# Kernel optimization log

Hardware: AMD Instinct MI355X
Metric: run time of the kernel (lower is better)

## Reference

```python
import jax, jax.numpy as jnp
import numpy as np

N_NODES = 65536
N_EDGES = 524288
N_GRAPHS = 512
G_NODES = 10000
NUM_DISEASES = 2000
IN_DIM = 128
HID = 256  # 2 * IN_DIM (z_emb concat feat)
D_FEAT = 512
C_FEAT = 512
MAX_Z = 4000


def setup_inputs() -> dict:
    key = jax.random.key(0)
    ks = jax.random.split(key, 20)
    rn = lambda k, shape: jax.random.normal(k, shape, dtype=jnp.float32) * 0.05
    return {
        "z": jax.random.randint(ks[0], (N_NODES,), 0, MAX_Z),
        "node_id": jnp.sort(jax.random.randint(ks[1], (N_NODES,), 0, G_NODES)),
        "src": jax.random.randint(ks[2], (N_EDGES,), 0, N_NODES),
        "dst": jax.random.randint(ks[3], (N_EDGES,), 0, N_NODES),
        "graph_ids": jnp.sort(jax.random.randint(ks[4], (N_NODES,), 0, N_GRAPHS)),
        "z_table": rn(ks[5], (MAX_Z, IN_DIM)),
        "d_feat_tab": rn(ks[6], (G_NODES, D_FEAT)),
        "c_feat_tab": rn(ks[7], (G_NODES, C_FEAT)),
        "Wd": rn(ks[8], (D_FEAT, IN_DIM)),
        "Wc": rn(ks[9], (C_FEAT, IN_DIM)),
        "gin_W1": rn(ks[10], (HID, HID)), "gin_b1": jnp.zeros((HID,), jnp.float32),
        "gin_W2": rn(ks[11], (HID, HID)), "gin_b2": jnp.zeros((HID,), jnp.float32),
        "sage_Wself": rn(ks[12], (HID, HID)),
        "sage_Wneigh": rn(ks[13], (HID, HID)),
        "sage_b": jnp.zeros((HID,), jnp.float32),
        "lin1_W": rn(ks[14], (HID, HID)), "lin1_b": jnp.zeros((HID,), jnp.float32),
        "lin2_W": rn(ks[15], (HID, 1)), "lin2_b": jnp.zeros((1,), jnp.float32),
    }


def reference(z, node_id, src, dst, graph_ids, z_table, d_feat_tab, c_feat_tab,
              Wd, Wc, gin_W1, gin_b1, gin_W2, gin_b2,
              sage_Wself, sage_Wneigh, sage_b, lin1_W, lin1_b, lin2_W, lin2_b):
    # --- input feature construction (Model.forward) ---
    z_emb = z_table[z]                               # [N, IN_DIM]
    d_proj = d_feat_tab[node_id] @ Wd                # d_fc (bias=False)
    c_proj = c_feat_tab[node_id] @ Wc                # c_fc (bias=False)
    disease = (node_id <= NUM_DISEASES)[:, None]
    # node_id is sorted -> masked concat order == node order
    feat = jnp.where(disease, d_proj, c_proj)        # [N, IN_DIM]
    x = jnp.concatenate([z_emb, feat], axis=1)       # [N, HID]
    # --- GINConv: sum aggregation, eps=0, mlp = Lin->ReLU->Lin ---
    agg = jax.ops.segment_sum(x[src], dst, num_segments=N_NODES)
    h = x + agg
    h = jax.nn.relu(h @ gin_W1 + gin_b1) @ gin_W2 + gin_b2
    # --- SAGEConv('mean'): fc_self(h) + fc_neigh(mean_neighbors) + bias ---
    deg = jax.ops.segment_sum(jnp.ones((N_EDGES,), h.dtype), dst, num_segments=N_NODES)
    mean_n = jax.ops.segment_sum(h[src], dst, num_segments=N_NODES) / jnp.maximum(deg, 1.0)[:, None]
    h = h @ sage_Wself + mean_n @ sage_Wneigh + sage_b
    # --- per-graph max pooling readout ---
    g = jax.ops.segment_max(h, graph_ids, num_segments=N_GRAPHS, indices_are_sorted=True)
    g = jnp.where(jnp.isfinite(g), g, 0.0)           # guard empty graphs
    # --- head: Linear -> ReLU -> (dropout p=0, eval) -> Linear ---
    h = jax.nn.relu(g @ lin1_W + lin1_b)
    return h @ lin2_W + lin2_b                       # [N_GRAPHS, 1]
```

## Files before the change

kernel.cpp:

```cpp
#include <hip/hip_runtime.h>
#include <hip/hip_bf16.h>

#define N_NODES     65536
#define N_EDGES     524288
#define N_GRAPHS    512
#define G_NODES_N   10000
#define NUM_DIS     2000
#define IN_DIM      128
#define HID         256
#define D_FEAT      512
#define POOL_SPLIT  8

typedef _Float16 half8 __attribute__((ext_vector_type(8)));
typedef _Float16 half4v __attribute__((ext_vector_type(4)));
typedef float    f32x4 __attribute__((ext_vector_type(4)));

typedef __attribute__((address_space(1))) const void as1_void;
typedef __attribute__((address_space(3))) void       as3_void;

__global__ __launch_bounds__(256) void wcvt_all_kernel(
    const float* __restrict__ W1, const float* __restrict__ W2,
    const float* __restrict__ Ws, const float* __restrict__ Wn,
    const float* __restrict__ Wd, const float* __restrict__ Wc,
    _Float16* __restrict__ W1T, _Float16* __restrict__ W2T,
    _Float16* __restrict__ WsT, _Float16* __restrict__ WnT,
    _Float16* __restrict__ WdT, _Float16* __restrict__ WcT)
{
    __shared__ float tile[64][65];
    const int b = blockIdx.x;
    const int mat = b >> 4, t = b & 15;
    const float* W; _Float16* T; int K, N, k0, n0;
    if (mat < 4) {
        K = HID; N = HID; k0 = (t >> 2) * 64; n0 = (t & 3) * 64;
        W = (mat == 0) ? W1 : (mat == 1) ? W2 : (mat == 2) ? Ws : Wn;
        T = (mat == 0) ? W1T : (mat == 1) ? W2T : (mat == 2) ? WsT : WnT;
    } else {
        K = D_FEAT; N = IN_DIM; k0 = (t >> 1) * 64; n0 = (t & 1) * 64;
        W = (mat == 4) ? Wd : Wc;
        T = (mat == 4) ? WdT : WcT;
    }
    const int tx = threadIdx.x & 63, ty = threadIdx.x >> 6;
    #pragma unroll
    for (int r = 0; r < 64; r += 4)
        tile[r + ty][tx] = W[(size_t)(k0 + r + ty) * N + n0 + tx];
    __syncthreads();
    #pragma unroll
    for (int c = 0; c < 64; c += 4)
        T[(size_t)(n0 + c + ty) * K + k0 + tx] = (_Float16)tile[tx][c + ty];
}

__global__ __launch_bounds__(256) void proj_mfma_kernel(
    const float* __restrict__ dtab, const float* __restrict__ ctab,
    const _Float16* __restrict__ WdT, const _Float16* __restrict__ WcT,
    _Float16* __restrict__ proj)
{
    __shared__ _Float16 Alds[128 * 40];
    __shared__ _Float16 Blds[128 * 40];
    const int blk = blockIdx.x;
    const float* tab; const _Float16* WT; int base, M, bm;
    if (blk < 16) { tab = dtab; WT = WdT; base = 0;           M = NUM_DIS + 1;             bm = blk * 128; }
    else          { tab = ctab; WT = WcT; base = NUM_DIS + 1; M = G_NODES_N - NUM_DIS - 1; bm = (blk - 16) * 128; }
    const int tid  = threadIdx.x;
    const int wave = tid >> 6, lane = tid & 63;
    const int q    = lane >> 4, l16 = lane & 15;
    const int mbase = (wave & 1) * 64, nbase = (wave >> 1) * 64;
    const int r = tid >> 1, s = tid & 1;

    f32x4 acc[4][4] = {};

    for (int kc = 0; kc < 16; ++kc) {
        const int k0 = kc * 32;
        const int arow = min(bm + r, M - 1);
        const float* gA = tab + (size_t)(base + arow) * D_FEAT + k0 + s * 16;
        const _Float16* gB = WT + (size_t)r * D_FEAT + k0 + s * 16;
        const float4 f0 = ((const float4*)gA)[0];
        const float4 f1 = ((const float4*)gA)[1];
        const float4 f2 = ((const float4*)gA)[2];
        const float4 f3 = ((const float4*)gA)[3];
        const half8 hb0 = *(const half8*)gB;
        const half8 hb1 = *(const half8*)(gB + 8);
        half8 h0, h1;
        h0[0]=(_Float16)f0.x; h0[1]=(_Float16)f0.y; h0[2]=(_Float16)f0.z; h0[3]=(_Float16)f0.w;
        h0[4]=(_Float16)f1.x; h0[5]=(_Float16)f1.y; h0[6]=(_Float16)f1.z; h0[7]=(_Float16)f1.w;
        h1[0]=(_Float16)f2.x; h1[1]=(_Float16)f2.y; h1[2]=(_Float16)f2.z; h1[3]=(_Float16)f2.w;
        h1[4]=(_Float16)f3.x; h1[5]=(_Float16)f3.y; h1[6]=(_Float16)f3.z; h1[7]=(_Float16)f3.w;
        __syncthreads();
        *(half8*)&Alds[r * 40 + s * 16]     = h0;
        *(half8*)&Alds[r * 40 + s * 16 + 8] = h1;
        *(half8*)&Blds[r * 40 + s * 16]     = hb0;
        *(half8*)&Blds[r * 40 + s * 16 + 8] = hb1;
        __syncthreads();
        half8 a[4], b[4];
        #pragma unroll
        for (int i = 0; i < 4; ++i)
            a[i] = *(const half8*)&Alds[(mbase + i * 16 + l16) * 40 + q * 8];
        #pragma unroll
        for (int j = 0; j < 4; ++j)
            b[j] = *(const half8*)&Blds[(nbase + j * 16 + l16) * 40 + q * 8];
        #pragma unroll
        for (int i = 0; i < 4; ++i)
            #pragma unroll
            for (int j = 0; j < 4; ++j)
                acc[i][j] = __builtin_amdgcn_mfma_f32_16x16x32_f16(a[i], b[j], acc[i][j], 0, 0, 0);
    }

    #pragma unroll
    for (int j = 0; j < 4; ++j) {
        const int colg = nbase + j * 16 + l16;
        #pragma unroll
        for (int i = 0; i < 4; ++i) {
            #pragma unroll
            for (int rr = 0; rr < 4; ++rr) {
                const int row = bm + mbase + i * 16 + q * 4 + rr;
                if (row < M)
                    proj[(size_t)(base + row) * IN_DIM + colg] = (_Float16)acc[i][j][rr];
            }
        }
    }
}

__global__ __launch_bounds__(256) void build_x_kernel(
    const int* __restrict__ z, const int* __restrict__ node_id,
    const float* __restrict__ z_table, const _Float16* __restrict__ proj,
    _Float16* __restrict__ X)
{
    const int t = blockIdx.x * 256 + threadIdx.x;
    const int node = t >> 6;
    const int q    = t & 63;
    half4v h;
    if (q < 32) {
        const float4 v = ((const float4*)(z_table + (size_t)z[node] * IN_DIM))[q];
        h[0] = (_Float16)v.x; h[1] = (_Float16)v.y;
        h[2] = (_Float16)v.z; h[3] = (_Float16)v.w;
    } else {
        h = *(const half4v*)(proj + (size_t)node_id[node] * IN_DIM + (q - 32) * 4);
    }
    *(half4v*)(X + (size_t)node * HID + q * 4) = h;
}

__global__ __launch_bounds__(256) void hist_kernel(
    const int* __restrict__ dst, int* __restrict__ cnt)
{
    const int e = blockIdx.x * 256 + threadIdx.x;
    if (e < N_EDGES) atomicAdd(&cnt[dst[e]], 1);
}

__global__ __launch_bounds__(256) void seg_sum_kernel(
    const int* __restrict__ cnt, int* __restrict__ seg)
{
    __shared__ int red[256];
    const int t = threadIdx.x;
    const int4 c = *(const int4*)(cnt + blockIdx.x * 1024 + t * 4);
    red[t] = c.x + c.y + c.z + c.w;
    __syncthreads();
    for (int s = 128; s > 0; s >>= 1) {
        if (t < s) red[t] += red[t + s];
        __syncthreads();
    }
    if (t == 0) seg[blockIdx.x] = red[0];
}

__global__ __launch_bounds__(64) void seg_scan_kernel(
    const int* __restrict__ seg, int* __restrict__ segoff,
    int* __restrict__ total_out)
{
    __shared__ int a[64], b[64];
    const int t = threadIdx.x;
    const int v = seg[t];
    a[t] = v;
    __syncthreads();
    int* in = a; int* out = b;
    for (int off = 1; off < 64; off <<= 1) {
        out[t] = in[t] + ((t >= off) ? in[t - off] : 0);
        __syncthreads();
        int* tmp = in; in = out; out = tmp;
    }
    segoff[t] = in[t] - v;
    if (t == 63) total_out[0] = in[63];
}

__global__ __launch_bounds__(256) void local_scan_kernel(
    const int* __restrict__ cnt, const int* __restrict__ segoff,
    int* __restrict__ row_ptr, int* __restrict__ fill)
{
    __shared__ int a[256], b[256];
    const int t = threadIdx.x;
    const int base = blockIdx.x * 1024 + t * 4;
    const int4 c = *(const int4*)(cnt + base);
    const int s = c.x + c.y + c.z + c.w;
    a[t] = s;
    __syncthreads();
    int* in = a; int* out = b;
    for (int off = 1; off < 256; off <<= 1) {
        out[t] = in[t] + ((t >= off) ? in[t - off] : 0);
        __syncthreads();
        int* tmp = in; in = out; out = tmp;
    }
    const int run = in[t] - s + segoff[blockIdx.x];
    int4 r;
    r.x = run; r.y = run + c.x; r.z = r.y + c.y; r.w = r.z + c.z;
    *(int4*)(row_ptr + base) = r;
    *(int4*)(fill + base) = r;
}

__global__ __launch_bounds__(256) void scatter_kernel(
    const int* __restrict__ src, const int* __restrict__ dst,
    int* __restrict__ fill, int* __restrict__ col)
{
    const int e = blockIdx.x * 256 + threadIdx.x;
    if (e < N_EDGES) {
        const int pos = atomicAdd(&fill[dst[e]], 1);
        col[pos] = src[e];
    }
}

__global__ __launch_bounds__(256) void csr_agg_kernel(
    const int* __restrict__ row_ptr, const int* __restrict__ col,
    const _Float16* __restrict__ F, const _Float16* __restrict__ Self,
    _Float16* __restrict__ OUT, const int mean_mode)
{
    const int t = blockIdx.x * 256 + threadIdx.x;
    const int d = t >> 5;
    const int q = t & 31;
    const int beg = row_ptr[d];
    const int end = row_ptr[d + 1];
    float acc[8] = {0.f,0.f,0.f,0.f,0.f,0.f,0.f,0.f};
    if (Self) {
        const half8 sv = *(const half8*)(Self + (size_t)d * HID + q * 8);
        #pragma unroll
        for (int i = 0; i < 8; ++i) acc[i] = (float)sv[i];
    }
    int e = beg;
    for (; e + 4 <= end; e += 4) {
        const int s0 = col[e],     s1 = col[e + 1];
        const int s2 = col[e + 2], s3 = col[e + 3];
        const half8 v0 = *(const half8*)(F + (size_t)s0 * HID + q * 8);
        const half8 v1 = *(const half8*)(F + (size_t)s1 * HID + q * 8);
        const half8 v2 = *(const half8*)(F + (size_t)s2 * HID + q * 8);
        const half8 v3 = *(const half8*)(F + (size_t)s3 * HID + q * 8);
        #pragma unroll
        for (int i = 0; i < 8; ++i)
            acc[i] += ((float)v0[i] + (float)v1[i]) + ((float)v2[i] + (float)v3[i]);
    }
    for (; e < end; ++e) {
        const half8 v0 = *(const half8*)(F + (size_t)col[e] * HID + q * 8);
        #pragma unroll
        for (int i = 0; i < 8; ++i) acc[i] += (float)v0[i];
    }
    if (mean_mode) {
        const float rs = 1.0f / fmaxf((float)(end - beg), 1.0f);
        #pragma unroll
        for (int i = 0; i < 8; ++i) acc[i] *= rs;
    }
    half8 o;
    #pragma unroll
    for (int i = 0; i < 8; ++i) o[i] = (_Float16)acc[i];
    *(half8*)(OUT + (size_t)d * HID + q * 8) = o;
}

__global__ __launch_bounds__(256) void mfma_gemm_kernel(
    const _Float16* __restrict__ A1, const _Float16* __restrict__ A2,
    const _Float16* __restrict__ B1T, const _Float16* __restrict__ B2T,
    const float* __restrict__ bias, _Float16* __restrict__ Ch, const int relu)
{
    __shared__ _Float16 Alds[128 * 32];
    __shared__ _Float16 Blds[128 * 32];
    const int bm   = blockIdx.x * 128;
    const int bn   = blockIdx.y * 128;
    const int tid  = threadIdx.x;
    const int wave = tid >> 6, lane = tid & 63;
    const int q    = lane >> 4, l16 = lane & 15;
    const int mbase = (wave & 1) * 64, nbase = (wave >> 1) * 64;

    f32x4 acc[4][4] = {};
    const int nchunks = A2 ? 16 : 8;

    for (int kc = 0; kc < nchunks; ++kc) {
        const int k0 = (kc & 7) * 32;
        const _Float16* Abase = (kc < 8) ? A1 : A2;
        const _Float16* Bbase = (kc < 8) ? B1T : B2T;
        __syncthreads();
        #pragma unroll
        for (int t = 0; t < 2; ++t) {
            const int i   = wave * 128 + t * 64 + lane;
            const int row = i >> 2, s = i & 3;
            const _Float16* gA = Abase + (size_t)(bm + row) * HID + k0 + s * 8;
            const _Float16* gB = Bbase + (size_t)(bn + row) * HID + k0 + s * 8;
            __builtin_amdgcn_global_load_lds(
                (as1_void*)gA, (as3_void*)&Alds[(wave * 128 + t * 64) * 8], 16, 0, 0);
            __builtin_amdgcn_global_load_lds(
                (as1_void*)gB, (as3_void*)&Blds[(wave * 128 + t * 64) * 8], 16, 0, 0);
        }
        __syncthreads();
        half8 a[4], b[4];
        #pragma unroll
        for (int i = 0; i < 4; ++i)
            a[i] = *(const half8*)&Alds[(mbase + i * 16 + l16) * 32 + q * 8];
        #pragma unroll
        for (int j = 0; j < 4; ++j)
            b[j] = *(const half8*)&Blds[(nbase + j * 16 + l16) * 32 + q * 8];
        #pragma unroll
        for (int i = 0; i < 4; ++i)
            #pragma unroll
            for (int j = 0; j < 4; ++j)
                acc[i][j] = __builtin_amdgcn_mfma_f32_16x16x32_f16(a[i], b[j], acc[i][j], 0, 0, 0);
    }

    #pragma unroll
    for (int j = 0; j < 4; ++j) {
        const int colg = bn + nbase + j * 16 + l16;
        const float bv = bias ? bias[colg] : 0.0f;
        #pragma unroll
        for (int i = 0; i < 4; ++i) {
            #pragma unroll
            for (int rr = 0; rr < 4; ++rr) {
                const int rowg = bm + mbase + i * 16 + q * 4 + rr;
                float v = acc[i][j][rr] + bv;
                if (relu) v = fmaxf(v, 0.0f);
                Ch[(size_t)rowg * HID + colg] = (_Float16)v;
            }
        }
    }
}

__global__ __launch_bounds__(256) void pool_part_kernel(
    const _Float16* __restrict__ H2, const int* __restrict__ gid,
    float* __restrict__ Gpart)
{
    const int g = blockIdx.y;
    const int sp = blockIdx.x;
    const int j = threadIdx.x;
    int lo = 0, hi = N_NODES;
    while (lo < hi) { const int mid = (lo + hi) >> 1; if (gid[mid] < g) lo = mid + 1; else hi = mid; }
    const int start = lo;
    hi = N_NODES;
    while (lo < hi) { const int mid = (lo + hi) >> 1; if (gid[mid] < g + 1) lo = mid + 1; else hi = mid; }
    const int end = lo;
    float m = -INFINITY;
    for (int i = start + sp; i < end; i += POOL_SPLIT)
        m = fmaxf(m, (float)H2[(size_t)i * HID + j]);
    Gpart[((size_t)g * POOL_SPLIT + sp) * HID + j] = m;
}

__global__ __launch_bounds__(256) void head_kernel(
    const float* __restrict__ Gpart,
    const float* __restrict__ W1, const float* __restrict__ b1,
    const float* __restrict__ W2, const float* __restrict__ b2,
    float* __restrict__ out)
{
    const int g = blockIdx.x;
    const int j = threadIdx.x;
    __shared__ float row[HID];
    __shared__ float red[HID];
    float m = -INFINITY;
    #pragma unroll
    for (int sp = 0; sp < POOL_SPLIT; ++sp)
        m = fmaxf(m, Gpart[((size_t)g * POOL_SPLIT + sp) * HID + j]);
    row[j] = (m == -INFINITY) ? 0.0f : m;
    __syncthreads();
    float acc = b1[j];
    #pragma unroll 8
    for (int k = 0; k < HID; ++k)
        acc = fmaf(row[k], W1[k * HID + j], acc);
    acc = fmaxf(acc, 0.f);
    red[j] = acc * W2[j];
    __syncthreads();
    for (int s = 128; s > 0; s >>= 1) {
        if (j < s) red[j] += red[j + s];
        __syncthreads();
    }
    if (j == 0) out[g] = red[0] + b2[0];
}

extern "C" void kernel_launch(void* const* d_in, const int* in_sizes, int n_in,
                              void* d_out, int out_size, void* d_ws, size_t ws_size,
                              hipStream_t stream)
{
    const int*   z         = (const int*)d_in[0];
    const int*   node_id   = (const int*)d_in[1];
    const int*   src       = (const int*)d_in[2];
    const int*   dst       = (const int*)d_in[3];
    const int*   graph_ids = (const int*)d_in[4];
    const float* z_table   = (const float*)d_in[5];
    const float* d_feat    = (const float*)d_in[6];
    const float* c_feat    = (const float*)d_in[7];
    const float* Wd        = (const float*)d_in[8];
    const float* Wc        = (const float*)d_in[9];
    const float* gin_W1    = (const float*)d_in[10];
    const float* gin_b1    = (const float*)d_in[11];
    const float* gin_W2    = (const float*)d_in[12];
    const float* gin_b2    = (const float*)d_in[13];
    const float* sage_Wself  = (const float*)d_in[14];
    const float* sage_Wneigh = (const float*)d_in[15];
    const float* sage_b    = (const float*)d_in[16];
    const float* lin1_W    = (const float*)d_in[17];
    const float* lin1_b    = (const float*)d_in[18];
    const float* lin2_W    = (const float*)d_in[19];
    const float* lin2_b    = (const float*)d_in[20];
    float* out = (float*)d_out;

    const size_t NH = (size_t)N_NODES * HID;
    char* wsb = (char*)d_ws;
    _Float16* bufA = (_Float16*)wsb;                     wsb += NH * 2;
    _Float16* AGGh = (_Float16*)wsb;                     wsb += NH * 2;
    _Float16* H1h  = (_Float16*)wsb;                     wsb += NH * 2;
    _Float16* projh= (_Float16*)wsb;                     wsb += (size_t)G_NODES_N * IN_DIM * 2;
    _Float16* W1T  = (_Float16*)wsb;                     wsb += HID * HID * 2;
    _Float16* W2T  = (_Float16*)wsb;                     wsb += HID * HID * 2;
    _Float16* WsT  = (_Float16*)wsb;                     wsb += HID * HID * 2;
    _Float16* WnT  = (_Float16*)wsb;                     wsb += HID * HID * 2;
    _Float16* WdT  = (_Float16*)wsb;                     wsb += D_FEAT * IN_DIM * 2;
    _Float16* WcT  = (_Float16*)wsb;                     wsb += D_FEAT * IN_DIM * 2;
    float* Gpart   = (float*)wsb;                        wsb += (size_t)N_GRAPHS * POOL_SPLIT * HID * 4;
    int* row_ptr   = (int*)wsb;                          wsb += (N_NODES + 4) * 4;
    int* cnt       = (int*)wsb;                          wsb += N_NODES * 4;
    int* fill      = (int*)wsb;                          wsb += N_NODES * 4;
    int* col       = (int*)wsb;                          wsb += N_EDGES * 4;
    int* seg       = (int*)wsb;                          wsb += 64 * 4;
    int* segoff    = (int*)wsb;                          wsb += 64 * 4;

    _Float16* Xh  = bufA;
    _Float16* Hh  = bufA;
    _Float16* H2h = H1h;

    hipMemsetAsync(cnt, 0, N_NODES * sizeof(int), stream);
    hist_kernel<<<N_EDGES / 256, 256, 0, stream>>>(dst, cnt);
    seg_sum_kernel<<<64, 256, 0, stream>>>(cnt, seg);
    seg_scan_kernel<<<1, 64, 0, stream>>>(seg, segoff, &row_ptr[N_NODES]);
    local_scan_kernel<<<64, 256, 0, stream>>>(cnt, segoff, row_ptr, fill);
    scatter_kernel<<<N_EDGES / 256, 256, 0, stream>>>(src, dst, fill, col);

    wcvt_all_kernel<<<96, 256, 0, stream>>>(gin_W1, gin_W2, sage_Wself, sage_Wneigh,
                                            Wd, Wc, W1T, W2T, WsT, WnT, WdT, WcT);

    proj_mfma_kernel<<<16 + 63, 256, 0, stream>>>(d_feat, c_feat, WdT, WcT, projh);

    build_x_kernel<<<(N_NODES * 64) / 256, 256, 0, stream>>>(z, node_id, z_table, projh, Xh);

    csr_agg_kernel<<<(N_NODES * 32) / 256, 256, 0, stream>>>(row_ptr, col, Xh, Xh, AGGh, 0);

    dim3 ggrid(N_NODES / 128, HID / 128);
    mfma_gemm_kernel<<<ggrid, 256, 0, stream>>>(AGGh, nullptr, W1T, nullptr, gin_b1, H1h, 1);
    mfma_gemm_kernel<<<ggrid, 256, 0, stream>>>(H1h, nullptr, W2T, nullptr, gin_b2, Hh, 0);

    csr_agg_kernel<<<(N_NODES * 32) / 256, 256, 0, stream>>>(row_ptr, col, Hh, nullptr, AGGh, 1);

    mfma_gemm_kernel<<<ggrid, 256, 0, stream>>>(Hh, AGGh, WsT, WnT, sage_b, H2h, 0);

    dim3 pgrid(POOL_SPLIT, N_GRAPHS);
    pool_part_kernel<<<pgrid, 256, 0, stream>>>(H2h, graph_ids, Gpart);
    head_kernel<<<N_GRAPHS, 256, 0, stream>>>(Gpart, lin1_W, lin1_b, lin2_W, lin2_b, out);
}
```

Measured before the change: 428.5 us.

## Fuse CSR neighbor aggregation into MFMA GEMM prologue with double-buffered weights

```diff
diff --git a/kernel.cpp b/kernel.cpp
--- a/kernel.cpp
+++ b/kernel.cpp
@@ -214,110 +214,128 @@
     }
 }
 
-__global__ __launch_bounds__(256) void csr_agg_kernel(
-    const int* __restrict__ row_ptr, const int* __restrict__ col,
-    const _Float16* __restrict__ F, const _Float16* __restrict__ Self,
-    _Float16* __restrict__ OUT, const int mean_mode)
-{
-    const int t = blockIdx.x * 256 + threadIdx.x;
-    const int d = t >> 5;
-    const int q = t & 31;
-    const int beg = row_ptr[d];
-    const int end = row_ptr[d + 1];
-    float acc[8] = {0.f,0.f,0.f,0.f,0.f,0.f,0.f,0.f};
-    if (Self) {
-        const half8 sv = *(const half8*)(Self + (size_t)d * HID + q * 8);
-        #pragma unroll
-        for (int i = 0; i < 8; ++i) acc[i] = (float)sv[i];
-    }
-    int e = beg;
-    for (; e + 4 <= end; e += 4) {
-        const int s0 = col[e],     s1 = col[e + 1];
-        const int s2 = col[e + 2], s3 = col[e + 3];
-        const half8 v0 = *(const half8*)(F + (size_t)s0 * HID + q * 8);
-        const half8 v1 = *(const half8*)(F + (size_t)s1 * HID + q * 8);
-        const half8 v2 = *(const half8*)(F + (size_t)s2 * HID + q * 8);
-        const half8 v3 = *(const half8*)(F + (size_t)s3 * HID + q * 8);
-        #pragma unroll
-        for (int i = 0; i < 8; ++i)
-            acc[i] += ((float)v0[i] + (float)v1[i]) + ((float)v2[i] + (float)v3[i]);
-    }
-    for (; e < end; ++e) {
-        const half8 v0 = *(const half8*)(F + (size_t)col[e] * HID + q * 8);
-        #pragma unroll
-        for (int i = 0; i < 8; ++i) acc[i] += (float)v0[i];
-    }
-    if (mean_mode) {
-        const float rs = 1.0f / fmaxf((float)(end - beg), 1.0f);
-        #pragma unroll
-        for (int i = 0; i < 8; ++i) acc[i] *= rs;
-    }
-    half8 o;
-    #pragma unroll
-    for (int i = 0; i < 8; ++i) o[i] = (_Float16)acc[i];
-    *(half8*)(OUT + (size_t)d * HID + q * 8) = o;
-}
-
-__global__ __launch_bounds__(256) void mfma_gemm_kernel(
-    const _Float16* __restrict__ A1, const _Float16* __restrict__ A2,
-    const _Float16* __restrict__ B1T, const _Float16* __restrict__ B2T,
-    const float* __restrict__ bias, _Float16* __restrict__ Ch, const int relu)
-{
-    __shared__ _Float16 Alds[128 * 32];
-    __shared__ _Float16 Blds[128 * 32];
-    const int bm   = blockIdx.x * 128;
-    const int bn   = blockIdx.y * 128;
+template<bool HAS_GATHER, bool HAS_GLOBAL, bool MEAN, bool SELF, int RELU>
+__global__ __launch_bounds__(256) void fused_gemm_kernel(
+    const int* __restrict__ row_ptr, const int* __restrict__ colv,
+    const _Float16* __restrict__ F,
+    const _Float16* __restrict__ Ag,
+    const _Float16* __restrict__ BgT,
+    const _Float16* __restrict__ BhT,
+    const float* __restrict__ bias, _Float16* __restrict__ C)
+{
+    __shared__ _Float16 AGGlds[HAS_GATHER ? 32 * 32 * 8 : 8];
+    __shared__ _Float16 Blds[2][4 * 256 * 8];
+    __shared__ _Float16 Alds[2][HAS_GLOBAL ? 4 * 32 * 8 : 8];
+
+    const int bm   = blockIdx.x * 32;
     const int tid  = threadIdx.x;
     const int wave = tid >> 6, lane = tid & 63;
     const int q    = lane >> 4, l16 = lane & 15;
-    const int mbase = (wave & 1) * 64, nbase = (wave >> 1) * 64;
-
-    f32x4 acc[4][4] = {};
-    const int nchunks = A2 ? 16 : 8;
-
-    for (int kc = 0; kc < nchunks; ++kc) {
-        const int k0 = (kc & 7) * 32;
-        const _Float16* Abase = (kc < 8) ? A1 : A2;
-        const _Float16* Bbase = (kc < 8) ? B1T : B2T;
-        __syncthreads();
-        #pragma unroll
-        for (int t = 0; t < 2; ++t) {
-            const int i   = wave * 128 + t * 64 + lane;
-            const int row = i >> 2, s = i & 3;
-            const _Float16* gA = Abase + (size_t)(bm + row) * HID + k0 + s * 8;
-            const _Float16* gB = Bbase + (size_t)(bn + row) * HID + k0 + s * 8;
-            __builtin_amdgcn_global_load_lds(
-                (as1_void*)gA, (as3_void*)&Alds[(wave * 128 + t * 64) * 8], 16, 0, 0);
-            __builtin_amdgcn_global_load_lds(
-                (as1_void*)gB, (as3_void*)&Blds[(wave * 128 + t * 64) * 8], 16, 0, 0);
-        }
-        __syncthreads();
-        half8 a[4], b[4];
-        #pragma unroll
-        for (int i = 0; i < 4; ++i)
-            a[i] = *(const half8*)&Alds[(mbase + i * 16 + l16) * 32 + q * 8];
+    const int nbase = wave * 64;
+    const int nglob = HAS_GLOBAL ? 8 : 0;
+    const int nch   = nglob + (HAS_GATHER ? 8 : 0);
+
+    auto stage = [&](int c, int buf) {
+        const int kc = (c < nglob) ? c : (c - nglob);
+        const int k0 = kc * 32;
+        const _Float16* Bt = (c < nglob) ? BgT : BhT;
+        #pragma unroll
+        for (int tt = 0; tt < 4; ++tt) {
+            const int seg = (wave * 4 + tt) * 64 + lane;
+            const int n = seg & 255, ks = seg >> 8;
+            const _Float16* g = Bt + (size_t)n * HID + k0 + ks * 8;
+            __builtin_amdgcn_global_load_lds((as1_void*)g,
+                (as3_void*)&Blds[buf][(wave * 4 + tt) * 64 * 8], 16, 0, 0);
+        }
+        if (HAS_GLOBAL && c < nglob && wave < 2) {
+            const int seg = wave * 64 + lane;
+            const int ks = seg >> 5, row = seg & 31;
+            const _Float16* g = Ag + (size_t)(bm + row) * HID + k0 + ks * 8;
+            __builtin_amdgcn_global_load_lds((as1_void*)g,
+                (as3_void*)&Alds[buf][wave * 64 * 8], 16, 0, 0);
+        }
+    };
+
+    stage(0, 0);
+
+    if (HAS_GATHER) {
+        const int r = tid >> 3, s = tid & 7;
+        const int gr = bm + r;
+        const int beg = row_ptr[gr], end = row_ptr[gr + 1];
+        float gacc[32];
+        #pragma unroll
+        for (int i = 0; i < 32; ++i) gacc[i] = 0.f;
+        if (SELF) {
+            const half8* sp = (const half8*)(F + (size_t)gr * HID + s * 32);
+            #pragma unroll
+            for (int u = 0; u < 4; ++u) {
+                const half8 v = sp[u];
+                #pragma unroll
+                for (int i = 0; i < 8; ++i) gacc[u * 8 + i] = (float)v[i];
+            }
+        }
+        for (int e = beg; e < end; ++e) {
+            const half8* p8 = (const half8*)(F + (size_t)colv[e] * HID + s * 32);
+            const half8 v0 = p8[0], v1 = p8[1], v2 = p8[2], v3 = p8[3];
+            #pragma unroll
+            for (int i = 0; i < 8; ++i) {
+                gacc[i]      += (float)v0[i];
+                gacc[8 + i]  += (float)v1[i];
+                gacc[16 + i] += (float)v2[i];
+                gacc[24 + i] += (float)v3[i];
+            }
+        }
+        if (MEAN) {
+            const float rs = 1.0f / fmaxf((float)(end - beg), 1.0f);
+            #pragma unroll
+            for (int i = 0; i < 32; ++i) gacc[i] *= rs;
+        }
+        #pragma unroll
+        for (int u = 0; u < 4; ++u) {
+            half8 o;
+            #pragma unroll
+            for (int i = 0; i < 8; ++i) o[i] = (_Float16)gacc[u * 8 + i];
+            *(half8*)&AGGlds[((s * 4 + u) * 32 + r) * 8] = o;
+        }
+    }
+    __syncthreads();
+
+    f32x4 cacc[2][4] = {};
+    int p = 0;
+    for (int c = 0; c < nch; ++c) {
+        if (c + 1 < nch) stage(c + 1, p ^ 1);
+        half8 a[2], b[4];
+        const bool gl = (c < nglob);
+        #pragma unroll
+        for (int i = 0; i < 2; ++i) {
+            const int row = i * 16 + l16;
+            if (gl) a[i] = *(const half8*)&Alds[p][(q * 32 + row) * 8];
+            else    a[i] = *(const half8*)&AGGlds[(((c - nglob) * 4 + q) * 32 + row) * 8];
+        }
         #pragma unroll
         for (int j = 0; j < 4; ++j)
-            b[j] = *(const half8*)&Blds[(nbase + j * 16 + l16) * 32 + q * 8];
-        #pragma unroll
-        for (int i = 0; i < 4; ++i)
+            b[j] = *(const half8*)&Blds[p][(q * 256 + nbase + j * 16 + l16) * 8];
+        #pragma unroll
+        for (int i = 0; i < 2; ++i)
             #pragma unroll
             for (int j = 0; j < 4; ++j)
-                acc[i][j] = __builtin_amdgcn_mfma_f32_16x16x32_f16(a[i], b[j], acc[i][j], 0, 0, 0);
+                cacc[i][j] = __builtin_amdgcn_mfma_f32_16x16x32_f16(a[i], b[j], cacc[i][j], 0, 0, 0);
+        __syncthreads();
+        p ^= 1;
     }
 
     #pragma unroll
     for (int j = 0; j < 4; ++j) {
-        const int colg = bn + nbase + j * 16 + l16;
-        const float bv = bias ? bias[colg] : 0.0f;
-        #pragma unroll
-        for (int i = 0; i < 4; ++i) {
+        const int colg = nbase + j * 16 + l16;
+        const float bv = bias[colg];
+        #pragma unroll
+        for (int i = 0; i < 2; ++i) {
             #pragma unroll
             for (int rr = 0; rr < 4; ++rr) {
-                const int rowg = bm + mbase + i * 16 + q * 4 + rr;
-                float v = acc[i][j][rr] + bv;
-                if (relu) v = fmaxf(v, 0.0f);
-                Ch[(size_t)rowg * HID + colg] = (_Float16)v;
+                const int rowg = bm + i * 16 + q * 4 + rr;
+                float v = cacc[i][j][rr] + bv;
+                if (RELU) v = fmaxf(v, 0.0f);
+                C[(size_t)rowg * HID + colg] = (_Float16)v;
             }
         }
     }
@@ -402,7 +420,6 @@
     const size_t NH = (size_t)N_NODES * HID;
     char* wsb = (char*)d_ws;
     _Float16* bufA = (_Float16*)wsb;                     wsb += NH * 2;
-    _Float16* AGGh = (_Float16*)wsb;                     wsb += NH * 2;
     _Float16* H1h  = (_Float16*)wsb;                     wsb += NH * 2;
     _Float16* projh= (_Float16*)wsb;                     wsb += (size_t)G_NODES_N * IN_DIM * 2;
     _Float16* W1T  = (_Float16*)wsb;                     wsb += HID * HID * 2;
@@ -437,15 +454,14 @@
 
     build_x_kernel<<<(N_NODES * 64) / 256, 256, 0, stream>>>(z, node_id, z_table, projh, Xh);
 
-    csr_agg_kernel<<<(N_NODES * 32) / 256, 256, 0, stream>>>(row_ptr, col, Xh, Xh, AGGh, 0);
-
-    dim3 ggrid(N_NODES / 128, HID / 128);
-    mfma_gemm_kernel<<<ggrid, 256, 0, stream>>>(AGGh, nullptr, W1T, nullptr, gin_b1, H1h, 1);
-    mfma_gemm_kernel<<<ggrid, 256, 0, stream>>>(H1h, nullptr, W2T, nullptr, gin_b2, Hh, 0);
-
-    csr_agg_kernel<<<(N_NODES * 32) / 256, 256, 0, stream>>>(row_ptr, col, Hh, nullptr, AGGh, 1);
-
-    mfma_gemm_kernel<<<ggrid, 256, 0, stream>>>(Hh, AGGh, WsT, WnT, sage_b, H2h, 0);
+    fused_gemm_kernel<true, false, false, true, 1><<<N_NODES / 32, 256, 0, stream>>>(
+        row_ptr, col, Xh, nullptr, nullptr, W1T, gin_b1, H1h);
+
+    fused_gemm_kernel<false, true, false, false, 0><<<N_NODES / 32, 256, 0, stream>>>(
+        nullptr, nullptr, nullptr, H1h, W2T, nullptr, gin_b2, Hh);
+
+    fused_gemm_kernel<true, true, true, false, 0><<<N_NODES / 32, 256, 0, stream>>>(
+        row_ptr, col, Hh, Hh, WsT, WnT, sage_b, H2h);
 
     dim3 pgrid(POOL_SPLIT, N_GRAPHS);
     pool_part_kernel<<<pgrid, 256, 0, stream>>>(H2h, graph_ids, Gpart);
```

After: 493.7 us. 1.15x slower.

## Fuse input build, GIN aggregation and both GIN MLP GEMMs into one kernel

Applied to the files above, without the earlier changes.

```diff
diff --git a/kernel.cpp b/kernel.cpp
--- a/kernel.cpp
+++ b/kernel.cpp
@@ -19,25 +19,25 @@
 typedef __attribute__((address_space(3))) void       as3_void;
 
 __global__ __launch_bounds__(256) void wcvt_all_kernel(
-    const float* __restrict__ W1, const float* __restrict__ W2,
     const float* __restrict__ Ws, const float* __restrict__ Wn,
     const float* __restrict__ Wd, const float* __restrict__ Wc,
-    _Float16* __restrict__ W1T, _Float16* __restrict__ W2T,
     _Float16* __restrict__ WsT, _Float16* __restrict__ WnT,
     _Float16* __restrict__ WdT, _Float16* __restrict__ WcT)
 {
     __shared__ float tile[64][65];
     const int b = blockIdx.x;
-    const int mat = b >> 4, t = b & 15;
     const float* W; _Float16* T; int K, N, k0, n0;
-    if (mat < 4) {
+    if (b < 32) {
+        const int mat = b >> 4, t = b & 15;
         K = HID; N = HID; k0 = (t >> 2) * 64; n0 = (t & 3) * 64;
-        W = (mat == 0) ? W1 : (mat == 1) ? W2 : (mat == 2) ? Ws : Wn;
-        T = (mat == 0) ? W1T : (mat == 1) ? W2T : (mat == 2) ? WsT : WnT;
+        W = (mat == 0) ? Ws : Wn;
+        T = (mat == 0) ? WsT : WnT;
     } else {
+        const int bb = b - 32;
+        const int mat = bb >> 4, t = bb & 15;
         K = D_FEAT; N = IN_DIM; k0 = (t >> 1) * 64; n0 = (t & 1) * 64;
-        W = (mat == 4) ? Wd : Wc;
-        T = (mat == 4) ? WdT : WcT;
+        W = (mat == 0) ? Wd : Wc;
+        T = (mat == 0) ? WdT : WcT;
     }
     const int tx = threadIdx.x & 63, ty = threadIdx.x >> 6;
     #pragma unroll
@@ -47,6 +47,21 @@
     #pragma unroll
     for (int c = 0; c < 64; c += 4)
         T[(size_t)(n0 + c + ty) * K + k0 + tx] = (_Float16)tile[tx][c + ty];
+}
+
+__global__ __launch_bounds__(256) void wprep_kernel(
+    const float* __restrict__ W1, const float* __restrict__ W2,
+    _Float16* __restrict__ W12P)
+{
+    const int b = blockIdx.x;
+    const int mat = b >> 8;
+    const int k = b & 255;
+    const int n = threadIdx.x;
+    const float* W = mat ? W2 : W1;
+    const float v = W[(size_t)k * HID + n];
+    const size_t idx = (size_t)(mat * 8 + (k >> 5)) * 8192
+                     + (size_t)((((k >> 3) & 3) * 256 + n) * 8 + (k & 7));
+    W12P[idx] = (_Float16)v;
 }
 
 __global__ __launch_bounds__(256) void proj_mfma_kernel(
@@ -119,25 +134,6 @@
     }
 }
 
-__global__ __launch_bounds__(256) void build_x_kernel(
-    const int* __restrict__ z, const int* __restrict__ node_id,
-    const float* __restrict__ z_table, const _Float16* __restrict__ proj,
-    _Float16* __restrict__ X)
-{
-    const int t = blockIdx.x * 256 + threadIdx.x;
-    const int node = t >> 6;
-    const int q    = t & 63;
-    half4v h;
-    if (q < 32) {
-        const float4 v = ((const float4*)(z_table + (size_t)z[node] * IN_DIM))[q];
-        h[0] = (_Float16)v.x; h[1] = (_Float16)v.y;
-        h[2] = (_Float16)v.z; h[3] = (_Float16)v.w;
-    } else {
-        h = *(const half4v*)(proj + (size_t)node_id[node] * IN_DIM + (q - 32) * 4);
-    }
-    *(half4v*)(X + (size_t)node * HID + q * 4) = h;
-}
-
 __global__ __launch_bounds__(256) void hist_kernel(
     const int* __restrict__ dst, int* __restrict__ cnt)
 {
@@ -214,10 +210,140 @@
     }
 }
 
+__global__ __launch_bounds__(256) void gin_fused_kernel(
+    const int* __restrict__ row_ptr, const int* __restrict__ colv,
+    const int* __restrict__ z, const int* __restrict__ node_id,
+    const float* __restrict__ z_table, const _Float16* __restrict__ proj,
+    const _Float16* __restrict__ W12P,
+    const float* __restrict__ b1, const float* __restrict__ b2,
+    _Float16* __restrict__ H)
+{
+    __shared__ _Float16 Apanel[32 * 264];
+    __shared__ _Float16 Blds[2][8192];
+
+    const int bm   = blockIdx.x * 32;
+    const int tid  = threadIdx.x;
+    const int wave = tid >> 6, lane = tid & 63;
+    const int q    = lane >> 4, l16 = lane & 15;
+    const int nbase = wave * 64;
+
+    auto stage = [&](int c, int buf) {
+        const _Float16* src = W12P + (size_t)c * 8192;
+        #pragma unroll
+        for (int tt = 0; tt < 4; ++tt) {
+            const int seg = (wave * 4 + tt) * 64 + lane;
+            __builtin_amdgcn_global_load_lds((as1_void*)(src + seg * 8),
+                (as3_void*)&Blds[buf][(wave * 4 + tt) * 64 * 8], 16, 0, 0);
+        }
+    };
+
+    stage(0, 0);
+
+    {
+        const int r = tid >> 3, p = tid & 7;
+        const int gr = bm + r;
+        const int beg = row_ptr[gr], end = row_ptr[gr + 1];
+        float za[16], pa[16];
+        {
+            const int zv = z[gr], nv = node_id[gr];
+            const float4* zp = (const float4*)(z_table + (size_t)zv * IN_DIM + p * 16);
+            const half8*  pp = (const half8*) (proj    + (size_t)nv * IN_DIM + p * 16);
+            #pragma unroll
+            for (int u = 0; u < 4; ++u) {
+                const float4 v = zp[u];
+                za[u*4+0]=v.x; za[u*4+1]=v.y; za[u*4+2]=v.z; za[u*4+3]=v.w;
+            }
+            #pragma unroll
+            for (int u = 0; u < 2; ++u) {
+                const half8 v = pp[u];
+                #pragma unroll
+                for (int i = 0; i < 8; ++i) pa[u*8+i] = (float)v[i];
+            }
+        }
+        for (int e = beg; e < end; ++e) {
+            const int s = colv[e];
+            const int zv = z[s], nv = node_id[s];
+            const float4* zp = (const float4*)(z_table + (size_t)zv * IN_DIM + p * 16);
+            const half8*  pp = (const half8*) (proj    + (size_t)nv * IN_DIM + p * 16);
+            #pragma unroll
+            for (int u = 0; u < 4; ++u) {
+                const float4 v = zp[u];
+                za[u*4+0]+=v.x; za[u*4+1]+=v.y; za[u*4+2]+=v.z; za[u*4+3]+=v.w;
+            }
+            #pragma unroll
+            for (int u = 0; u < 2; ++u) {
+                const half8 v = pp[u];
+                #pragma unroll
+                for (int i = 0; i < 8; ++i) pa[u*8+i] += (float)v[i];
+            }
+        }
+        half8 oz0, oz1, op0, op1;
+        #pragma unroll
+        for (int i = 0; i < 8; ++i) {
+            oz0[i] = (_Float16)za[i];     oz1[i] = (_Float16)za[8 + i];
+            op0[i] = (_Float16)pa[i];     op1[i] = (_Float16)pa[8 + i];
+        }
+        *(half8*)&Apanel[r * 264 + p * 16]           = oz0;
+        *(half8*)&Apanel[r * 264 + p * 16 + 8]       = oz1;
+        *(half8*)&Apanel[r * 264 + 128 + p * 16]     = op0;
+        *(half8*)&Apanel[r * 264 + 128 + p * 16 + 8] = op1;
+    }
+    __syncthreads();
+
+    f32x4 acc[2][4] = {};
+    int pb = 0;
+    for (int c = 0; c < 16; ++c) {
+        if (c + 1 < 16) stage(c + 1, pb ^ 1);
+        if (c == 8) {
+            #pragma unroll
+            for (int j = 0; j < 4; ++j) {
+                const int colg = nbase + j * 16 + l16;
+                const float bv = b1[colg];
+                #pragma unroll
+                for (int i = 0; i < 2; ++i)
+                    #pragma unroll
+                    for (int rr = 0; rr < 4; ++rr) {
+                        const float v = fmaxf(acc[i][j][rr] + bv, 0.0f);
+                        Apanel[(i * 16 + q * 4 + rr) * 264 + colg] = (_Float16)v;
+                        acc[i][j][rr] = 0.0f;
+                    }
+            }
+            __syncthreads();
+        }
+        const int kl = (c & 7) * 32;
+        half8 a[2], b[4];
+        #pragma unroll
+        for (int i = 0; i < 2; ++i)
+            a[i] = *(const half8*)&Apanel[(i * 16 + l16) * 264 + kl + q * 8];
+        #pragma unroll
+        for (int j = 0; j < 4; ++j)
+            b[j] = *(const half8*)&Blds[pb][(q * 256 + nbase + j * 16 + l16) * 8];
+        #pragma unroll
+        for (int i = 0; i < 2; ++i)
+            #pragma unroll
+            for (int j = 0; j < 4; ++j)
+                acc[i][j] = __builtin_amdgcn_mfma_f32_16x16x32_f16(a[i], b[j], acc[i][j], 0, 0, 0);
+        __syncthreads();
+        pb ^= 1;
+    }
+
+    #pragma unroll
+    for (int j = 0; j < 4; ++j) {
+        const int colg = nbase + j * 16 + l16;
+        const float bv = b2[colg];
+        #pragma unroll
+        for (int i = 0; i < 2; ++i)
+            #pragma unroll
+            for (int rr = 0; rr < 4; ++rr) {
+                const int rowg = bm + i * 16 + q * 4 + rr;
+                H[(size_t)rowg * HID + colg] = (_Float16)(acc[i][j][rr] + bv);
+            }
+    }
+}
+
 __global__ __launch_bounds__(256) void csr_agg_kernel(
     const int* __restrict__ row_ptr, const int* __restrict__ col,
-    const _Float16* __restrict__ F, const _Float16* __restrict__ Self,
-    _Float16* __restrict__ OUT, const int mean_mode)
+    const _Float16* __restrict__ F, _Float16* __restrict__ OUT)
 {
     const int t = blockIdx.x * 256 + threadIdx.x;
     const int d = t >> 5;
@@ -225,11 +351,6 @@
     const int beg = row_ptr[d];
     const int end = row_ptr[d + 1];
     float acc[8] = {0.f,0.f,0.f,0.f,0.f,0.f,0.f,0.f};
-    if (Self) {
-        const half8 sv = *(const half8*)(Self + (size_t)d * HID + q * 8);
-        #pragma unroll
-        for (int i = 0; i < 8; ++i) acc[i] = (float)sv[i];
-    }
     int e = beg;
     for (; e + 4 <= end; e += 4) {
         const int s0 = col[e],     s1 = col[e + 1];
@@ -247,21 +368,17 @@
         #pragma unroll
         for (int i = 0; i < 8; ++i) acc[i] += (float)v0[i];
     }
-    if (mean_mode) {
-        const float rs = 1.0f / fmaxf((float)(end - beg), 1.0f);
-        #pragma unroll
-        for (int i = 0; i < 8; ++i) acc[i] *= rs;
-    }
+    const float rs = 1.0f / fmaxf((float)(end - beg), 1.0f);
     half8 o;
     #pragma unroll
-    for (int i = 0; i < 8; ++i) o[i] = (_Float16)acc[i];
+    for (int i = 0; i < 8; ++i) o[i] = (_Float16)(acc[i] * rs);
     *(half8*)(OUT + (size_t)d * HID + q * 8) = o;
 }
 
 __global__ __launch_bounds__(256) void mfma_gemm_kernel(
     const _Float16* __restrict__ A1, const _Float16* __restrict__ A2,
     const _Float16* __restrict__ B1T, const _Float16* __restrict__ B2T,
-    const float* __restrict__ bias, _Float16* __restrict__ Ch, const int relu)
+    const float* __restrict__ bias, _Float16* __restrict__ Ch)
 {
     __shared__ _Float16 Alds[128 * 32];
     __shared__ _Float16 Blds[128 * 32];
@@ -273,9 +390,8 @@
     const int mbase = (wave & 1) * 64, nbase = (wave >> 1) * 64;
 
     f32x4 acc[4][4] = {};
-    const int nchunks = A2 ? 16 : 8;
-
-    for (int kc = 0; kc < nchunks; ++kc) {
+
+    for (int kc = 0; kc < 16; ++kc) {
         const int k0 = (kc & 7) * 32;
         const _Float16* Abase = (kc < 8) ? A1 : A2;
         const _Float16* Bbase = (kc < 8) ? B1T : B2T;
@@ -309,15 +425,13 @@
     #pragma unroll
     for (int j = 0; j < 4; ++j) {
         const int colg = bn + nbase + j * 16 + l16;
-        const float bv = bias ? bias[colg] : 0.0f;
+        const float bv = bias[colg];
         #pragma unroll
         for (int i = 0; i < 4; ++i) {
             #pragma unroll
             for (int rr = 0; rr < 4; ++rr) {
                 const int rowg = bm + mbase + i * 16 + q * 4 + rr;
-                float v = acc[i][j][rr] + bv;
-                if (relu) v = fmaxf(v, 0.0f);
-                Ch[(size_t)rowg * HID + colg] = (_Float16)v;
+                Ch[(size_t)rowg * HID + colg] = (_Float16)(acc[i][j][rr] + bv);
             }
         }
     }
@@ -401,12 +515,11 @@
 
     const size_t NH = (size_t)N_NODES * HID;
     char* wsb = (char*)d_ws;
-    _Float16* bufA = (_Float16*)wsb;                     wsb += NH * 2;
+    _Float16* Hh   = (_Float16*)wsb;                     wsb += NH * 2;
     _Float16* AGGh = (_Float16*)wsb;                     wsb += NH * 2;
-    _Float16* H1h  = (_Float16*)wsb;                     wsb += NH * 2;
+    _Float16* H2h  = (_Float16*)wsb;                     wsb += NH * 2;
     _Float16* projh= (_Float16*)wsb;                     wsb += (size_t)G_NODES_N * IN_DIM * 2;
-    _Float16* W1T  = (_Float16*)wsb;                     wsb += HID * HID * 2;
-    _Float16* W2T  = (_Float16*)wsb;                     wsb += HID * HID * 2;
+    _Float16* W12P = (_Float16*)wsb;                     wsb += 16 * 8192 * 2;
     _Float16* WsT  = (_Float16*)wsb;                     wsb += HID * HID * 2;
     _Float16* WnT  = (_Float16*)wsb;                     wsb += HID * HID * 2;
     _Float16* WdT  = (_Float16*)wsb;                     wsb += D_FEAT * IN_DIM * 2;
@@ -419,10 +532,6 @@
     int* seg       = (int*)wsb;                          wsb += 64 * 4;
     int* segoff    = (int*)wsb;                          wsb += 64 * 4;
 
-    _Float16* Xh  = bufA;
-    _Float16* Hh  = bufA;
-    _Float16* H2h = H1h;
-
     hipMemsetAsync(cnt, 0, N_NODES * sizeof(int), stream);
     hist_kernel<<<N_EDGES / 256, 256, 0, stream>>>(dst, cnt);
     seg_sum_kernel<<<64, 256, 0, stream>>>(cnt, seg);
@@ -430,22 +539,19 @@
     local_scan_kernel<<<64, 256, 0, stream>>>(cnt, segoff, row_ptr, fill);
     scatter_kernel<<<N_EDGES / 256, 256, 0, stream>>>(src, dst, fill, col);
 
-    wcvt_all_kernel<<<96, 256, 0, stream>>>(gin_W1, gin_W2, sage_Wself, sage_Wneigh,
-                                            Wd, Wc, W1T, W2T, WsT, WnT, WdT, WcT);
+    wcvt_all_kernel<<<64, 256, 0, stream>>>(sage_Wself, sage_Wneigh, Wd, Wc,
+                                            WsT, WnT, WdT, WcT);
+    wprep_kernel<<<512, 256, 0, stream>>>(gin_W1, gin_W2, W12P);
 
     proj_mfma_kernel<<<16 + 63, 256, 0, stream>>>(d_feat, c_feat, WdT, WcT, projh);
 
-    build_x_kernel<<<(N_NODES * 64) / 256, 256, 0, stream>>>(z, node_id, z_table, projh, Xh);
-
-    csr_agg_kernel<<<(N_NODES * 32) / 256, 256, 0, stream>>>(row_ptr, col, Xh, Xh, AGGh, 0);
+    gin_fused_kernel<<<N_NODES / 32, 256, 0, stream>>>(
+        row_ptr, col, z, node_id, z_table, projh, W12P, gin_b1, gin_b2, Hh);
+
+    csr_agg_kernel<<<(N_NODES * 32) / 256, 256, 0, stream>>>(row_ptr, col, Hh, AGGh);
 
     dim3 ggrid(N_NODES / 128, HID / 128);
-    mfma_gemm_kernel<<<ggrid, 256, 0, stream>>>(AGGh, nullptr, W1T, nullptr, gin_b1, H1h, 1);
-    mfma_gemm_kernel<<<ggrid, 256, 0, stream>>>(H1h, nullptr, W2T, nullptr, gin_b2, Hh, 0);
-
-    csr_agg_kernel<<<(N_NODES * 32) / 256, 256, 0, stream>>>(row_ptr, col, Hh, nullptr, AGGh, 1);
-
-    mfma_gemm_kernel<<<ggrid, 256, 0, stream>>>(Hh, AGGh, WsT, WnT, sage_b, H2h, 0);
+    mfma_gemm_kernel<<<ggrid, 256, 0, stream>>>(Hh, AGGh, WsT, WnT, sage_b, H2h);
 
     dim3 pgrid(POOL_SPLIT, N_GRAPHS);
     pool_part_kernel<<<pgrid, 256, 0, stream>>>(H2h, graph_ids, Gpart);
```

Result: faster. 390.3 us (-8.9%).
